# Performance work log

Hardware: AMD Instinct MI355X
Metric: run time of the kernel (lower is better)

## Reference

```python
import jax, jax.numpy as jnp
import numpy as np

N, E, EL = 65536, 1048576, 2097152
IN, H, OUT = 32, 64, 64


def setup_inputs() -> dict:
    key = jax.random.key(0)
    ks = jax.random.split(key, 20)
    inp = {
        "x": jax.random.normal(ks[0], (N, IN), dtype=jnp.float32),
        "edge_index": jax.random.randint(ks[1], (2, E), 0, N, dtype=jnp.int64),
        "edge_weight": jax.random.uniform(ks[2], (E,), dtype=jnp.float32),
        "edge_label_index": jax.random.randint(ks[3], (2, EL), 0, N, dtype=jnp.int64),
    }
    dims = [(IN, H), (H, H), (H, H), (H, H), (H, H), (H, OUT)]
    for i, (di, do) in enumerate(dims):
        scale = (2.0 / (di + do)) ** 0.5
        inp[f"w{i+1}"] = jax.random.normal(ks[4 + i], (di, do), dtype=jnp.float32) * scale
        inp[f"b{i+1}"] = jnp.zeros((do,), dtype=jnp.float32)
    return inp


def _gcn_norm(edge_index, edge_weight, num_nodes):
    # PyG GCNConv default: add self-loops (weight 1), symmetric normalization
    src, dst = edge_index[0], edge_index[1]
    loop = jnp.arange(num_nodes, dtype=edge_index.dtype)
    src_f = jnp.concatenate([src, loop])
    dst_f = jnp.concatenate([dst, loop])
    w_f = jnp.concatenate([edge_weight, jnp.ones((num_nodes,), edge_weight.dtype)])
    deg = jax.ops.segment_sum(w_f, dst_f, num_segments=num_nodes)
    dinv = jnp.where(deg > 0, jax.lax.rsqrt(jnp.where(deg > 0, deg, 1.0)), 0.0)
    norm = dinv[src_f] * w_f * dinv[dst_f]  # [E+N]
    return src_f, dst_f, norm


def _gcn_layer(x, W, b, src_f, dst_f, norm, num_nodes):
    h = x @ W  # transform first, then propagate (PyG GCNConv order)
    msg = norm[:, None] * h[src_f]  # gather + scale along edges
    out = jax.ops.segment_sum(msg, dst_f, num_segments=num_nodes)  # scatter-add
    return out + b


def reference(x, edge_index, edge_weight, edge_label_index,
              w1, b1, w2, b2, w3, b3, w4, b4, w5, b5, w6, b6):
    num_nodes = x.shape[0]
    src_f, dst_f, norm = _gcn_norm(edge_index, edge_weight, num_nodes)
    h = x
    for W, b in [(w1, b1), (w2, b2), (w3, b3), (w4, b4), (w5, b5)]:
        h = jax.nn.relu(_gcn_layer(h, W, b, src_f, dst_f, norm, num_nodes))
        # dropout = identity in deterministic reference
    encoded = _gcn_layer(h, w6, b6, src_f, dst_f, norm, num_nodes)
    # decode: elementwise dot over labeled edge pairs
    decoded = (encoded[edge_label_index[0]] * encoded[edge_label_index[1]]).sum(axis=1)
    return decoded
```

## Files before the change

kernel.cpp:

```cpp
#include <hip/hip_runtime.h>
#include <hip/hip_fp16.h>

#define N_NODES 65536
#define N_EDGES 1048576
#define N_LABEL 2097152
#define DIM_IN 32
#define DIM_H 64

typedef short short8 __attribute__((ext_vector_type(8)));
typedef float floatx4 __attribute__((ext_vector_type(4)));


__global__ void k_init(unsigned long long* __restrict__ packed) {
    int v = blockIdx.x * blockDim.x + threadIdx.x;
    packed[v] = 0ull;
}

__global__ void k_cnt(const int* __restrict__ ei, const float* __restrict__ w,
                      unsigned long long* __restrict__ packed,
                      unsigned short* __restrict__ rank) {
    int e = blockIdx.x * blockDim.x + threadIdx.x;
    int d = ei[N_EDGES + e];
    unsigned fx = __float2uint_rn(w[e] * 16777216.f);
    unsigned long long old = atomicAdd(&packed[d], (1ull << 32) | (unsigned long long)fx);
    rank[e] = (unsigned short)(old >> 32);
}

__global__ void k_scan1(const int2* __restrict__ packed, int* __restrict__ blksum) {
    int tid = threadIdx.x;
    const int2* p = packed + blockIdx.x * 1024 + tid * 4;
    int s = p[0].y + p[1].y + p[2].y + p[3].y;
    for (int d = 1; d < 64; d <<= 1) s += __shfl_xor(s, d);
    __shared__ int wsum[4];
    if ((tid & 63) == 0) wsum[tid >> 6] = s;
    __syncthreads();
    if (tid == 0) blksum[blockIdx.x] = wsum[0] + wsum[1] + wsum[2] + wsum[3];
}

__global__ void k_scan2(int* __restrict__ blksum) {
    if (threadIdx.x == 0) {
        int run = 0;
        for (int i = 0; i < 64; ++i) { int t = blksum[i]; blksum[i] = run; run += t; }
    }
}

__global__ void k_scan3(const int2* __restrict__ packed, const int* __restrict__ blksum,
                        int* __restrict__ offs) {
    int tid = threadIdx.x, bid = blockIdx.x;
    const int2* p = packed + bid * 1024 + tid * 4;
    int c0 = p[0].y, c1 = p[1].y, c2 = p[2].y, c3 = p[3].y;
    int s = c0 + c1 + c2 + c3;
    int lane = tid & 63, wid = tid >> 6;
    int sc = s;
    for (int d = 1; d < 64; d <<= 1) {
        int t = __shfl_up(sc, d);
        if (lane >= d) sc += t;
    }
    __shared__ int wsum[4];
    if (lane == 63) wsum[wid] = sc;
    __syncthreads();
    int base = blksum[bid];
    for (int w2 = 0; w2 < wid; ++w2) base += wsum[w2];
    int ex = base + sc - s;
    int idx = bid * 1024 + tid * 4;
    int o0 = ex, o1 = o0 + c0, o2 = o1 + c1, o3 = o2 + c2;
    offs[idx] = o0; offs[idx + 1] = o1; offs[idx + 2] = o2; offs[idx + 3] = o3;
    if (bid == 63 && tid == 255) offs[N_NODES] = o3 + c3;
}

__global__ void k_dinv(const uint2* __restrict__ packed, float* __restrict__ dinv) {
    int v = blockIdx.x * blockDim.x + threadIdx.x;
    float deg = 1.0f + (float)packed[v].x * (1.f / 16777216.f);
    dinv[v] = rsqrtf(deg);
}

__global__ void k_fill(const int* __restrict__ ei, const float* __restrict__ w,
                       const float* __restrict__ dinv, const int* __restrict__ offs,
                       const unsigned short* __restrict__ rank, int2* __restrict__ csr_se) {
    int e = blockIdx.x * blockDim.x + threadIdx.x;
    int s = ei[e];
    int d = ei[N_EDGES + e];
    int pos = offs[d] + rank[e];
    float nm = dinv[s] * w[e] * dinv[d];
    csr_se[pos] = make_int2(s, __float_as_int(nm));
}


__global__ void k_cast_x(const float* __restrict__ x, __half* __restrict__ xh) {
    int gid = blockIdx.x * 256 + threadIdx.x;
    xh[gid] = __float2half(x[gid]);
}


template <int K>
__global__ void __launch_bounds__(256) k_agg(
        const int* __restrict__ offs, const int2* __restrict__ csr_se,
        const __half* __restrict__ h, const float* __restrict__ dinv,
        float* __restrict__ agg) {
    constexpr int LPE = K / 8;
    constexpr int EPI = 64 / LPE;

    int tid = threadIdx.x;
    int v = blockIdx.x * 4 + (tid >> 6);
    int lane = tid & 63;
    int sub = lane % LPE;
    int g   = lane / LPE;

    float a[8] = {0.f, 0.f, 0.f, 0.f, 0.f, 0.f, 0.f, 0.f};

    if (g == 0) {
        float dv = dinv[v];
        float sl = dv * dv;
        uint4 rv = *(const uint4*)(h + (size_t)v * K + sub * 8);
        const __half2* hp = (const __half2*)&rv;
#pragma unroll
        for (int i = 0; i < 4; ++i) {
            float2 f = __half22float2(hp[i]);
            a[2 * i]     += sl * f.x;
            a[2 * i + 1] += sl * f.y;
        }
    }

    int j0 = __builtin_amdgcn_readfirstlane(offs[v]);
    int j1 = __builtin_amdgcn_readfirstlane(offs[v + 1]);

    for (int jm = j0; jm < j1; jm += 64) {
        int mi = jm + lane;
        int2 md = csr_se[mi < j1 ? mi : j1 - 1];
        if (mi >= j1) md.y = 0;
        int nwin = j1 - jm;
        if (nwin > 64) nwin = 64;
        for (int t = 0; t * EPI < nwin; ++t) {
            int we = t * EPI + g;
            int src = __shfl(md.x, we);
            float nm = __int_as_float(__shfl(md.y, we));
            uint4 rv = *(const uint4*)(h + (size_t)src * K + sub * 8);
            const __half2* hp = (const __half2*)&rv;
#pragma unroll
            for (int i = 0; i < 4; ++i) {
                float2 f = __half22float2(hp[i]);
                a[2 * i]     += nm * f.x;
                a[2 * i + 1] += nm * f.y;
            }
        }
    }

#pragma unroll
    for (int st = LPE; st < 64; st <<= 1) {
#pragma unroll
        for (int i = 0; i < 8; ++i) a[i] += __shfl_xor(a[i], st);
    }

    if (lane < LPE) {
        float* dst = agg + (size_t)v * K + lane * 8;
        *(float4*)(dst)     = make_float4(a[0], a[1], a[2], a[3]);
        *(float4*)(dst + 4) = make_float4(a[4], a[5], a[6], a[7]);
    }
}


__device__ __forceinline__ unsigned short f32_bf16(float f) {
    unsigned u = __float_as_uint(f);
    unsigned r = u + 0x7FFFu + ((u >> 16) & 1u);
    return (unsigned short)(r >> 16);
}
__device__ __forceinline__ float bf16_f32(unsigned short h) {
    return __uint_as_float(((unsigned)h) << 16);
}

template <int KIN, bool RELU>
__global__ void __launch_bounds__(256) k_gemm_mfma(
        const float* __restrict__ agg, const float* __restrict__ W,
        const float* __restrict__ b, __half* __restrict__ out) {
    constexpr int KC = KIN / 32;
    constexpr int NT = N_NODES / 16;
    __shared__ float Wl[KIN * 64];
    int tid = threadIdx.x;
    for (int i = tid; i < KIN * 64; i += 256) Wl[i] = W[i];
    __syncthreads();

    int lane = tid & 63;
    int l15 = lane & 15, l4 = lane >> 4;

    short8 whi[4][KC], wlo[4][KC];
#pragma unroll
    for (int ct = 0; ct < 4; ++ct)
#pragma unroll
        for (int kc = 0; kc < KC; ++kc)
#pragma unroll
            for (int j = 0; j < 8; ++j) {
                float wv = Wl[(kc * 32 + l4 * 8 + j) * 64 + ct * 16 + l15];
                unsigned short hi = f32_bf16(wv);
                unsigned short lo = f32_bf16(wv - bf16_f32(hi));
                whi[ct][kc][j] = (short)hi;
                wlo[ct][kc][j] = (short)lo;
            }
    float bias[4];
#pragma unroll
    for (int ct = 0; ct < 4; ++ct) bias[ct] = b[ct * 16 + l15];

    int wave_id = blockIdx.x * 4 + (tid >> 6);
    for (int tile = wave_id; tile < NT; tile += 2048) {
        int r0 = tile * 16;
        const float* arow = agg + (size_t)(r0 + l15) * KIN + l4 * 8;
        short8 ahi[KC], alo[KC];
#pragma unroll
        for (int kc = 0; kc < KC; ++kc) {
            float4 f0 = *(const float4*)(arow + kc * 32);
            float4 f1 = *(const float4*)(arow + kc * 32 + 4);
            float fv[8] = {f0.x, f0.y, f0.z, f0.w, f1.x, f1.y, f1.z, f1.w};
#pragma unroll
            for (int j = 0; j < 8; ++j) {
                unsigned short hi = f32_bf16(fv[j]);
                unsigned short lo = f32_bf16(fv[j] - bf16_f32(hi));
                ahi[kc][j] = (short)hi;
                alo[kc][j] = (short)lo;
            }
        }
        floatx4 acc[4] = {{0.f,0.f,0.f,0.f},{0.f,0.f,0.f,0.f},{0.f,0.f,0.f,0.f},{0.f,0.f,0.f,0.f}};
#pragma unroll
        for (int ct = 0; ct < 4; ++ct)
#pragma unroll
            for (int kc = 0; kc < KC; ++kc) {
                acc[ct] = __builtin_amdgcn_mfma_f32_16x16x32_bf16(ahi[kc], whi[ct][kc], acc[ct], 0, 0, 0);
                acc[ct] = __builtin_amdgcn_mfma_f32_16x16x32_bf16(ahi[kc], wlo[ct][kc], acc[ct], 0, 0, 0);
                acc[ct] = __builtin_amdgcn_mfma_f32_16x16x32_bf16(alo[kc], whi[ct][kc], acc[ct], 0, 0, 0);
            }
#pragma unroll
        for (int ct = 0; ct < 4; ++ct)
#pragma unroll
            for (int r = 0; r < 4; ++r) {
                float o = acc[ct][r] + bias[ct];
                if (RELU) o = fmaxf(o, 0.f);
                out[(size_t)(r0 + l4 * 4 + r) * 64 + ct * 16 + l15] = __float2half(o);
            }
    }
}


__device__ __forceinline__ float dot8h(uint4 ua, uint4 ub) {
    const __half2* pa = (const __half2*)&ua;
    const __half2* pb = (const __half2*)&ub;
    float s = 0.f;
#pragma unroll
    for (int i = 0; i < 4; ++i) {
        float2 fa = __half22float2(pa[i]);
        float2 fb = __half22float2(pb[i]);
        s += fa.x * fb.x + fa.y * fb.y;
    }
    return s;
}

__global__ void __launch_bounds__(256) k_decode(
        const int* __restrict__ eli, const __half* __restrict__ enc,
        float* __restrict__ out) {
    int gid = blockIdx.x * 256 + threadIdx.x;
    int p = gid >> 3;
    int c8 = gid & 7;
    int a = eli[p];
    int b = eli[N_LABEL + p];
    uint4 ua = *(const uint4*)(enc + (size_t)a * 64 + c8 * 8);
    uint4 ub = *(const uint4*)(enc + (size_t)b * 64 + c8 * 8);
    float s = dot8h(ua, ub);
    s += __shfl_xor(s, 1, 8);
    s += __shfl_xor(s, 2, 8);
    s += __shfl_xor(s, 4, 8);
    if (c8 == 0) out[p] = s;
}


extern "C" void kernel_launch(void* const* d_in, const int* in_sizes, int n_in,
                              void* d_out, int out_size, void* d_ws, size_t ws_size,
                              hipStream_t stream) {
    const float* x   = (const float*)d_in[0];
    const int*   ei  = (const int*)d_in[1];
    const float* ew  = (const float*)d_in[2];
    const int*   eli = (const int*)d_in[3];
    const float* W[6] = {(const float*)d_in[4],  (const float*)d_in[6],
                         (const float*)d_in[8],  (const float*)d_in[10],
                         (const float*)d_in[12], (const float*)d_in[14]};
    const float* B[6] = {(const float*)d_in[5],  (const float*)d_in[7],
                         (const float*)d_in[9],  (const float*)d_in[11],
                         (const float*)d_in[13], (const float*)d_in[15]};

    char* ws = (char*)d_ws;
    unsigned long long* packed = (unsigned long long*)ws;  ws += (size_t)N_NODES * 8;
    float*          dinv    = (float*)ws;           ws += N_NODES * 4;
    int*            offs    = (int*)ws;             ws += (N_NODES + 16) * 4;
    int*            blksum  = (int*)ws;             ws += 256 * 4;
    unsigned short* rank    = (unsigned short*)ws;  ws += (size_t)N_EDGES * 2;
    int2*           csr_se  = (int2*)ws;            ws += (size_t)N_EDGES * 8;
    __half*         xh      = (__half*)ws;          ws += (size_t)N_NODES * DIM_IN * 2;
    float*          aggF    = (float*)ws;           ws += (size_t)N_NODES * 64 * 4;
    __half*         hA      = (__half*)ws;          ws += (size_t)N_NODES * 64 * 2;
    __half*         hB      = (__half*)ws;

    const int BS = 256;
    const int gAgg = N_NODES / 4;
    const int gGemm = 512;

    k_init <<<N_NODES / BS, BS, 0, stream>>>(packed);
    k_cnt  <<<N_EDGES / BS, BS, 0, stream>>>(ei, ew, packed, rank);
    k_scan1<<<64, BS, 0, stream>>>((const int2*)packed, blksum);
    k_scan2<<<1, 64, 0, stream>>>(blksum);
    k_scan3<<<64, BS, 0, stream>>>((const int2*)packed, blksum, offs);
    k_dinv <<<N_NODES / BS, BS, 0, stream>>>((const uint2*)packed, dinv);
    k_fill <<<N_EDGES / BS, BS, 0, stream>>>(ei, ew, dinv, offs, rank, csr_se);

    k_cast_x<<<N_NODES * DIM_IN / BS, BS, 0, stream>>>(x, xh);

    k_agg<DIM_IN><<<gAgg, BS, 0, stream>>>(offs, csr_se, xh, dinv, aggF);
    k_gemm_mfma<DIM_IN, true><<<gGemm, BS, 0, stream>>>(aggF, W[0], B[0], hA);

    k_agg<DIM_H><<<gAgg, BS, 0, stream>>>(offs, csr_se, hA, dinv, aggF);
    k_gemm_mfma<DIM_H, true><<<gGemm, BS, 0, stream>>>(aggF, W[1], B[1], hB);
    k_agg<DIM_H><<<gAgg, BS, 0, stream>>>(offs, csr_se, hB, dinv, aggF);
    k_gemm_mfma<DIM_H, true><<<gGemm, BS, 0, stream>>>(aggF, W[2], B[2], hA);
    k_agg<DIM_H><<<gAgg, BS, 0, stream>>>(offs, csr_se, hA, dinv, aggF);
    k_gemm_mfma<DIM_H, true><<<gGemm, BS, 0, stream>>>(aggF, W[3], B[3], hB);
    k_agg<DIM_H><<<gAgg, BS, 0, stream>>>(offs, csr_se, hB, dinv, aggF);
    k_gemm_mfma<DIM_H, true><<<gGemm, BS, 0, stream>>>(aggF, W[4], B[4], hA);

    k_agg<DIM_H><<<gAgg, BS, 0, stream>>>(offs, csr_se, hA, dinv, aggF);
    k_gemm_mfma<DIM_H, false><<<gGemm, BS, 0, stream>>>(aggF, W[5], B[5], hB);

    k_decode<<<N_LABEL * 8 / BS, BS, 0, stream>>>(eli, hB, (float*)d_out);
}
```

Baseline: 413.6 us.

## Factor symmetric GCN normalization into per-node scaling and fold dinv into scan

Splits the per-edge norm dinv[s]*w*dinv[d] into a pre-scale of node features by dinv (done in the cast and GEMM epilogues) and a post-scale of aggregated rows by dinv. The CSR fill then stores raw edge weights and no longer does two random dinv gathers per edge. The separate dinv kernel is merged into scan3, removing one launch. Risk: fp16-stored features now carry a dinv factor, which slightly changes rounding.

```diff
diff --git a/kernel.cpp b/kernel.cpp
--- a/kernel.cpp
+++ b/kernel.cpp
@@ -45,10 +45,11 @@
 }
 
 __global__ void k_scan3(const int2* __restrict__ packed, const int* __restrict__ blksum,
-                        int* __restrict__ offs) {
+                        int* __restrict__ offs, float* __restrict__ dinv) {
     int tid = threadIdx.x, bid = blockIdx.x;
     const int2* p = packed + bid * 1024 + tid * 4;
-    int c0 = p[0].y, c1 = p[1].y, c2 = p[2].y, c3 = p[3].y;
+    int2 e0 = p[0], e1 = p[1], e2 = p[2], e3 = p[3];
+    int c0 = e0.y, c1 = e1.y, c2 = e2.y, c3 = e3.y;
     int s = c0 + c1 + c2 + c3;
     int lane = tid & 63, wid = tid >> 6;
     int sc = s;
@@ -66,29 +67,29 @@
     int o0 = ex, o1 = o0 + c0, o2 = o1 + c1, o3 = o2 + c2;
     offs[idx] = o0; offs[idx + 1] = o1; offs[idx + 2] = o2; offs[idx + 3] = o3;
     if (bid == 63 && tid == 255) offs[N_NODES] = o3 + c3;
-}
-
-__global__ void k_dinv(const uint2* __restrict__ packed, float* __restrict__ dinv) {
-    int v = blockIdx.x * blockDim.x + threadIdx.x;
-    float deg = 1.0f + (float)packed[v].x * (1.f / 16777216.f);
-    dinv[v] = rsqrtf(deg);
+    const float FXI = 1.f / 16777216.f;
+    dinv[idx]     = rsqrtf(1.f + (float)(unsigned)e0.x * FXI);
+    dinv[idx + 1] = rsqrtf(1.f + (float)(unsigned)e1.x * FXI);
+    dinv[idx + 2] = rsqrtf(1.f + (float)(unsigned)e2.x * FXI);
+    dinv[idx + 3] = rsqrtf(1.f + (float)(unsigned)e3.x * FXI);
 }
 
 __global__ void k_fill(const int* __restrict__ ei, const float* __restrict__ w,
-                       const float* __restrict__ dinv, const int* __restrict__ offs,
-                       const unsigned short* __restrict__ rank, int2* __restrict__ csr_se) {
+                       const int* __restrict__ offs, const unsigned short* __restrict__ rank,
+                       int2* __restrict__ csr_se) {
     int e = blockIdx.x * blockDim.x + threadIdx.x;
     int s = ei[e];
     int d = ei[N_EDGES + e];
     int pos = offs[d] + rank[e];
-    float nm = dinv[s] * w[e] * dinv[d];
-    csr_se[pos] = make_int2(s, __float_as_int(nm));
-}
-
-
-__global__ void k_cast_x(const float* __restrict__ x, __half* __restrict__ xh) {
+    csr_se[pos] = make_int2(s, __float_as_int(w[e]));
+}
+
+
+__global__ void k_cast_x(const float* __restrict__ x, const float* __restrict__ dinv,
+                         __half* __restrict__ xh) {
     int gid = blockIdx.x * 256 + threadIdx.x;
-    xh[gid] = __float2half(x[gid]);
+    int v = gid >> 5;
+    xh[gid] = __float2half(x[gid] * dinv[v]);
 }
 
 
@@ -109,15 +110,13 @@
     float a[8] = {0.f, 0.f, 0.f, 0.f, 0.f, 0.f, 0.f, 0.f};
 
     if (g == 0) {
-        float dv = dinv[v];
-        float sl = dv * dv;
         uint4 rv = *(const uint4*)(h + (size_t)v * K + sub * 8);
         const __half2* hp = (const __half2*)&rv;
 #pragma unroll
         for (int i = 0; i < 4; ++i) {
             float2 f = __half22float2(hp[i]);
-            a[2 * i]     += sl * f.x;
-            a[2 * i + 1] += sl * f.y;
+            a[2 * i]     += f.x;
+            a[2 * i + 1] += f.y;
         }
     }
 
@@ -133,14 +132,14 @@
         for (int t = 0; t * EPI < nwin; ++t) {
             int we = t * EPI + g;
             int src = __shfl(md.x, we);
-            float nm = __int_as_float(__shfl(md.y, we));
+            float wv = __int_as_float(__shfl(md.y, we));
             uint4 rv = *(const uint4*)(h + (size_t)src * K + sub * 8);
             const __half2* hp = (const __half2*)&rv;
 #pragma unroll
             for (int i = 0; i < 4; ++i) {
                 float2 f = __half22float2(hp[i]);
-                a[2 * i]     += nm * f.x;
-                a[2 * i + 1] += nm * f.y;
+                a[2 * i]     += wv * f.x;
+                a[2 * i + 1] += wv * f.y;
             }
         }
     }
@@ -152,9 +151,10 @@
     }
 
     if (lane < LPE) {
+        float dv = dinv[v];
         float* dst = agg + (size_t)v * K + lane * 8;
-        *(float4*)(dst)     = make_float4(a[0], a[1], a[2], a[3]);
-        *(float4*)(dst + 4) = make_float4(a[4], a[5], a[6], a[7]);
+        *(float4*)(dst)     = make_float4(dv * a[0], dv * a[1], dv * a[2], dv * a[3]);
+        *(float4*)(dst + 4) = make_float4(dv * a[4], dv * a[5], dv * a[6], dv * a[7]);
     }
 }
 
@@ -168,10 +168,11 @@
     return __uint_as_float(((unsigned)h) << 16);
 }
 
-template <int KIN, bool RELU>
+template <int KIN, bool RELU, bool SCALE>
 __global__ void __launch_bounds__(256) k_gemm_mfma(
         const float* __restrict__ agg, const float* __restrict__ W,
-        const float* __restrict__ b, __half* __restrict__ out) {
+        const float* __restrict__ b, const float* __restrict__ dinv,
+        __half* __restrict__ out) {
     constexpr int KC = KIN / 32;
     constexpr int NT = N_NODES / 16;
     __shared__ float Wl[KIN * 64];
@@ -230,9 +231,11 @@
         for (int ct = 0; ct < 4; ++ct)
 #pragma unroll
             for (int r = 0; r < 4; ++r) {
+                int row = r0 + l4 * 4 + r;
                 float o = acc[ct][r] + bias[ct];
                 if (RELU) o = fmaxf(o, 0.f);
-                out[(size_t)(r0 + l4 * 4 + r) * 64 + ct * 16 + l15] = __float2half(o);
+                if (SCALE) o *= dinv[row];
+                out[(size_t)row * 64 + ct * 16 + l15] = __float2half(o);
             }
     }
 }
@@ -303,26 +306,25 @@
     k_cnt  <<<N_EDGES / BS, BS, 0, stream>>>(ei, ew, packed, rank);
     k_scan1<<<64, BS, 0, stream>>>((const int2*)packed, blksum);
     k_scan2<<<1, 64, 0, stream>>>(blksum);
-    k_scan3<<<64, BS, 0, stream>>>((const int2*)packed, blksum, offs);
-    k_dinv <<<N_NODES / BS, BS, 0, stream>>>((const uint2*)packed, dinv);
-    k_fill <<<N_EDGES / BS, BS, 0, stream>>>(ei, ew, dinv, offs, rank, csr_se);
-
-    k_cast_x<<<N_NODES * DIM_IN / BS, BS, 0, stream>>>(x, xh);
+    k_scan3<<<64, BS, 0, stream>>>((const int2*)packed, blksum, offs, dinv);
+    k_fill <<<N_EDGES / BS, BS, 0, stream>>>(ei, ew, offs, rank, csr_se);
+
+    k_cast_x<<<N_NODES * DIM_IN / BS, BS, 0, stream>>>(x, dinv, xh);
 
     k_agg<DIM_IN><<<gAgg, BS, 0, stream>>>(offs, csr_se, xh, dinv, aggF);
-    k_gemm_mfma<DIM_IN, true><<<gGemm, BS, 0, stream>>>(aggF, W[0], B[0], hA);
+    k_gemm_mfma<DIM_IN, true, true><<<gGemm, BS, 0, stream>>>(aggF, W[0], B[0], dinv, hA);
 
     k_agg<DIM_H><<<gAgg, BS, 0, stream>>>(offs, csr_se, hA, dinv, aggF);
-    k_gemm_mfma<DIM_H, true><<<gGemm, BS, 0, stream>>>(aggF, W[1], B[1], hB);
+    k_gemm_mfma<DIM_H, true, true><<<gGemm, BS, 0, stream>>>(aggF, W[1], B[1], dinv, hB);
     k_agg<DIM_H><<<gAgg, BS, 0, stream>>>(offs, csr_se, hB, dinv, aggF);
-    k_gemm_mfma<DIM_H, true><<<gGemm, BS, 0, stream>>>(aggF, W[2], B[2], hA);
+    k_gemm_mfma<DIM_H, true, true><<<gGemm, BS, 0, stream>>>(aggF, W[2], B[2], dinv, hA);
     k_agg<DIM_H><<<gAgg, BS, 0, stream>>>(offs, csr_se, hA, dinv, aggF);
-    k_gemm_mfma<DIM_H, true><<<gGemm, BS, 0, stream>>>(aggF, W[3], B[3], hB);
+    k_gemm_mfma<DIM_H, true, true><<<gGemm, BS, 0, stream>>>(aggF, W[3], B[3], dinv, hB);
     k_agg<DIM_H><<<gAgg, BS, 0, stream>>>(offs, csr_se, hB, dinv, aggF);
-    k_gemm_mfma<DIM_H, true><<<gGemm, BS, 0, stream>>>(aggF, W[4], B[4], hA);
+    k_gemm_mfma<DIM_H, true, true><<<gGemm, BS, 0, stream>>>(aggF, W[4], B[4], dinv, hA);
 
     k_agg<DIM_H><<<gAgg, BS, 0, stream>>>(offs, csr_se, hA, dinv, aggF);
-    k_gemm_mfma<DIM_H, false><<<gGemm, BS, 0, stream>>>(aggF, W[5], B[5], hB);
+    k_gemm_mfma<DIM_H, false, false><<<gGemm, BS, 0, stream>>>(aggF, W[5], B[5], dinv, hB);
 
     k_decode<<<N_LABEL * 8 / BS, BS, 0, stream>>>(eli, hB, (float*)d_out);
 }
```

Result: no change. 416.6 us (+0.7%).
